# Kernel tuning notes

Hardware: AMD Instinct MI355X
Metric: run time of the kernel (lower is better)

## Reference

```python
import jax, jax.numpy as jnp
import numpy as np

EPS = 1e-12  # torch F.normalize eps

def _l2norm(v, axis):
    n = jnp.sqrt(jnp.sum(v * v, axis=axis, keepdims=True))
    return v / jnp.maximum(n, EPS)

def setup_inputs() -> dict:
    key = jax.random.key(0)
    k1, k2 = jax.random.split(key)
    B, N, D, K = 8, 2048, 128, 64
    x = jax.random.normal(k1, (B, N, D), dtype=jnp.float32)
    std1 = 1.0 / np.sqrt(K * D)
    centroids = jax.random.uniform(k2, (K, D), dtype=jnp.float32, minval=-std1, maxval=std1)
    return {"x": x, "centroids": centroids}

def reference(x, centroids):
    # x: [B, N, D], centroids: [K, D]
    B, N, D = x.shape
    K = centroids.shape[0]
    xn = _l2norm(x, axis=-1)                       # descriptor-wise L2 normalize
    res = xn[:, :, None, :] - centroids[None, None]  # [B, N, K, D]
    dist = jnp.sum(res * res, axis=-1)             # [B, N, K] squared distances
    assign = jax.nn.softmax(dist, axis=-1)         # softmax over clusters (NOTE: positive distances, as in source)
    vlad = jnp.einsum('bnk,bnkd->bkd', assign, res)  # weighted residual sum over N
    vlad = _l2norm(vlad, axis=2)                   # intra-normalization per cluster
    vlad = vlad.reshape(B, K * D)
    vlad = _l2norm(vlad, axis=1)                   # global L2 normalize
    return vlad
```

## Files before the change

### kernel.cpp

```cpp
#include <hip/hip_runtime.h>
#include <math.h>

#define BB 8
#define NN 2048
#define DD 128
#define KK 64
#define PP 32
#define NPB (NN / PP)

__global__ __launch_bounds__(256) void netvlad_k1(
    const float* __restrict__ x, const float* __restrict__ cent,
    float* __restrict__ part_acc, float* __restrict__ part_sA)
{
    const int b    = blockIdx.x >> 5;
    const int p    = blockIdx.x & 31;
    const int t    = threadIdx.x;
    const int kq   = t >> 3;
    const int pr   = t & 7;
    const int dbase = pr * 16;
    const int wave = t >> 6;
    const int lane = t & 63;
    const int half = (t >> 5) & 1;
    const int hl   = t & 31;

    __shared__ float xn[8][DD];
    __shared__ float eL[8][KK];
    __shared__ float rsum[8];

    int off[4];
    #pragma unroll
    for (int jj = 0; jj < 4; ++jj) off[jj] = dbase + (((jj + pr) & 3) << 2);

    float4 cA[4], cB[4];
    float cn2a = 0.f, cn2b = 0.f;
    #pragma unroll
    for (int jj = 0; jj < 4; ++jj) {
        cA[jj] = *(const float4*)(cent + (2 * kq) * DD + off[jj]);
        cB[jj] = *(const float4*)(cent + (2 * kq + 1) * DD + off[jj]);
        cn2a += cA[jj].x*cA[jj].x + cA[jj].y*cA[jj].y + cA[jj].z*cA[jj].z + cA[jj].w*cA[jj].w;
        cn2b += cB[jj].x*cB[jj].x + cB[jj].y*cB[jj].y + cB[jj].z*cB[jj].z + cB[jj].w*cB[jj].w;
    }
    #pragma unroll
    for (int m = 1; m < 8; m <<= 1) {
        cn2a += __shfl_xor(cn2a, m);
        cn2b += __shfl_xor(cn2b, m);
    }

    float4 acc0[4], acc1[4];
    #pragma unroll
    for (int jj = 0; jj < 4; ++jj) {
        acc0[jj] = make_float4(0.f, 0.f, 0.f, 0.f);
        acc1[jj] = make_float4(0.f, 0.f, 0.f, 0.f);
    }
    float sA0 = 0.f, sA1 = 0.f;

    const float* xb = x + ((size_t)b * NN + (size_t)p * NPB) * DD;

    for (int it = 0; it < NPB / 8; ++it) {
        __syncthreads();

        {
            const int i = wave * 2 + half;
            const float* xp = xb + (size_t)(it * 8 + i) * DD + hl * 4;
            float4 v = *(const float4*)xp;
            float ss = v.x*v.x + v.y*v.y + v.z*v.z + v.w*v.w;
            #pragma unroll
            for (int m = 1; m < 32; m <<= 1) ss += __shfl_xor(ss, m);
            const float rn = 1.0f / fmaxf(sqrtf(ss), 1e-12f);
            *(float4*)(&xn[i][hl * 4]) = make_float4(v.x*rn, v.y*rn, v.z*rn, v.w*rn);
        }
        __syncthreads();

        float e0[8], e1[8];
        #pragma unroll
        for (int i = 0; i < 8; ++i) {
            float S0 = 0.f, S1 = 0.f;
            #pragma unroll
            for (int jj = 0; jj < 4; ++jj) {
                float4 v = *(const float4*)(&xn[i][off[jj]]);
                S0 += v.x*cA[jj].x + v.y*cA[jj].y + v.z*cA[jj].z + v.w*cA[jj].w;
                S1 += v.x*cB[jj].x + v.y*cB[jj].y + v.z*cB[jj].z + v.w*cB[jj].w;
            }
            #pragma unroll
            for (int m = 1; m < 8; m <<= 1) {
                S0 += __shfl_xor(S0, m);
                S1 += __shfl_xor(S1, m);
            }
            e0[i] = __expf(cn2a - 2.f * S0);
            e1[i] = __expf(cn2b - 2.f * S1);
            if (pr == 0) *(float2*)(&eL[i][2 * kq]) = make_float2(e0[i], e1[i]);
        }
        __syncthreads();

        #pragma unroll
        for (int rep = 0; rep < 2; ++rep) {
            const int i = wave * 2 + rep;
            float e = eL[i][lane];
            #pragma unroll
            for (int m = 1; m < 64; m <<= 1) e += __shfl_xor(e, m);
            if (lane == 0) rsum[i] = 1.0f / e;
        }
        __syncthreads();

        #pragma unroll
        for (int i = 0; i < 8; ++i) {
            const float r = rsum[i];
            const float a0 = e0[i] * r, a1 = e1[i] * r;
            sA0 += a0; sA1 += a1;
            #pragma unroll
            for (int jj = 0; jj < 4; ++jj) {
                float4 v = *(const float4*)(&xn[i][off[jj]]);
                acc0[jj].x += a0*v.x; acc0[jj].y += a0*v.y; acc0[jj].z += a0*v.z; acc0[jj].w += a0*v.w;
                acc1[jj].x += a1*v.x; acc1[jj].y += a1*v.y; acc1[jj].z += a1*v.z; acc1[jj].w += a1*v.w;
            }
        }
    }

    const size_t base = (size_t)(b * PP + p) * KK * DD;
    #pragma unroll
    for (int jj = 0; jj < 4; ++jj) {
        *(float4*)(part_acc + base + (2 * kq) * DD + off[jj])     = acc0[jj];
        *(float4*)(part_acc + base + (2 * kq + 1) * DD + off[jj]) = acc1[jj];
    }
    if (pr == 0) {
        part_sA[(b * PP + p) * KK + 2 * kq]     = sA0;
        part_sA[(b * PP + p) * KK + 2 * kq + 1] = sA1;
    }
}

__global__ __launch_bounds__(128) void netvlad_k2(
    const float* __restrict__ cent, const float* __restrict__ part_acc,
    const float* __restrict__ part_sA, float* __restrict__ out,
    float* __restrict__ gnorm)
{
    const int b = blockIdx.x >> 6;
    const int k = blockIdx.x & 63;
    const int d = threadIdx.x;

    float sAt = 0.f;
    #pragma unroll
    for (int p = 0; p < PP; ++p) sAt += part_sA[(b * PP + p) * KK + k];

    float v = 0.f;
    #pragma unroll 8
    for (int p = 0; p < PP; ++p)
        v += part_acc[(size_t)(b * PP + p) * KK * DD + k * DD + d];
    v -= cent[k * DD + d] * sAt;

    float ss = v * v;
    #pragma unroll
    for (int m = 1; m < 64; m <<= 1) ss += __shfl_xor(ss, m);
    __shared__ float s2[2];
    if ((d & 63) == 0) s2[d >> 6] = ss;
    __syncthreads();
    const float tot = s2[0] + s2[1];
    const float rn = 1.0f / fmaxf(sqrtf(tot), 1e-12f);
    out[(size_t)b * KK * DD + k * DD + d] = v * rn;

    if (d == 0) atomicAdd(&gnorm[b], tot * rn * rn);
}

__global__ __launch_bounds__(256) void netvlad_k3(
    float* __restrict__ out, const float* __restrict__ gnorm)
{
    const int b = blockIdx.x >> 3;
    const int chunk = blockIdx.x & 7;
    const float rs = 1.0f / fmaxf(sqrtf(gnorm[b]), 1e-12f);
    float4* p = (float4*)(out + (size_t)b * KK * DD) + chunk * 256 + threadIdx.x;
    float4 v = *p;
    v.x *= rs; v.y *= rs; v.z *= rs; v.w *= rs;
    *p = v;
}

extern "C" void kernel_launch(void* const* d_in, const int* in_sizes, int n_in,
                              void* d_out, int out_size, void* d_ws, size_t ws_size,
                              hipStream_t stream) {
    const float* x    = (const float*)d_in[0];
    const float* cent = (const float*)d_in[1];
    float* out = (float*)d_out;

    char* ws = (char*)d_ws;
    float* gnorm    = (float*)ws;
    float* part_sA  = (float*)(ws + 4096);
    float* part_acc = (float*)(ws + 4096 + 65536);

    hipMemsetAsync(gnorm, 0, BB * sizeof(float), stream);

    netvlad_k1<<<dim3(BB * PP), dim3(256), 0, stream>>>(x, cent, part_acc, part_sA);
    netvlad_k2<<<dim3(BB * KK), dim3(128), 0, stream>>>(cent, part_acc, part_sA, out, gnorm);
    netvlad_k3<<<dim3(64), dim3(256), 0, stream>>>(out, gnorm);
}
```

Baseline: 106.3 us.

## Split N across more blocks, vectorize partial reduction, drop global-norm pass

The N dimension is split into 128 partitions instead of 32, so the main kernel launches four times as many blocks, and launch bounds request higher occupancy. The reduction kernel now sums partials with float4 loads, splitting the partition range across four thread groups and combining them through shared memory. The global L2 pass, its atomic and the memset are removed by using a constant 1/8 scale, since each of the 64 intra-normalized clusters has unit norm. In exchange, partial-accumulator traffic grows fourfold, and the constant scale is wrong if any cluster vector has zero norm.

Result: faster. 98.87 us (-7.0%).

```diff
diff --git a/kernel.cpp b/kernel.cpp
--- a/kernel.cpp
+++ b/kernel.cpp
@@ -5,15 +5,15 @@
 #define NN 2048
 #define DD 128
 #define KK 64
-#define PP 32
+#define PP 128
 #define NPB (NN / PP)
 
-__global__ __launch_bounds__(256) void netvlad_k1(
+__global__ __launch_bounds__(256, 4) void netvlad_k1(
     const float* __restrict__ x, const float* __restrict__ cent,
     float* __restrict__ part_acc, float* __restrict__ part_sA)
 {
-    const int b    = blockIdx.x >> 5;
-    const int p    = blockIdx.x & 31;
+    const int b    = blockIdx.x >> 7;
+    const int p    = blockIdx.x & 127;
     const int t    = threadIdx.x;
     const int kq   = t >> 3;
     const int pr   = t & 7;
@@ -130,46 +130,52 @@
 
 __global__ __launch_bounds__(128) void netvlad_k2(
     const float* __restrict__ cent, const float* __restrict__ part_acc,
-    const float* __restrict__ part_sA, float* __restrict__ out,
-    float* __restrict__ gnorm)
+    const float* __restrict__ part_sA, float* __restrict__ out)
 {
-    const int b = blockIdx.x >> 6;
-    const int k = blockIdx.x & 63;
-    const int d = threadIdx.x;
+    const int b  = blockIdx.x >> 6;
+    const int k  = blockIdx.x & 63;
+    const int t  = threadIdx.x;
+    const int d4 = t & 31;
+    const int ps = t >> 5;
 
-    float sAt = 0.f;
-    #pragma unroll
-    for (int p = 0; p < PP; ++p) sAt += part_sA[(b * PP + p) * KK + k];
+    __shared__ float sAL[2];
+    {
+        float sA = part_sA[(b * PP + t) * KK + k];
+        #pragma unroll
+        for (int m = 1; m < 64; m <<= 1) sA += __shfl_xor(sA, m);
+        if ((t & 63) == 0) sAL[t >> 6] = sA;
+    }
 
-    float v = 0.f;
+    float4 acc = make_float4(0.f, 0.f, 0.f, 0.f);
+    const float* base = part_acc + ((size_t)(b * PP) * KK + k) * DD + d4 * 4;
     #pragma unroll 8
-    for (int p = 0; p < PP; ++p)
-        v += part_acc[(size_t)(b * PP + p) * KK * DD + k * DD + d];
-    v -= cent[k * DD + d] * sAt;
+    for (int pp = 0; pp < 32; ++pp) {
+        const float4 v = *(const float4*)(base + (size_t)(ps * 32 + pp) * KK * DD);
+        acc.x += v.x; acc.y += v.y; acc.z += v.z; acc.w += v.w;
+    }
 
-    float ss = v * v;
-    #pragma unroll
-    for (int m = 1; m < 64; m <<= 1) ss += __shfl_xor(ss, m);
-    __shared__ float s2[2];
-    if ((d & 63) == 0) s2[d >> 6] = ss;
+    __shared__ float4 red[4][32];
+    red[ps][d4] = acc;
     __syncthreads();
-    const float tot = s2[0] + s2[1];
-    const float rn = 1.0f / fmaxf(sqrtf(tot), 1e-12f);
-    out[(size_t)b * KK * DD + k * DD + d] = v * rn;
+    const float sAt = sAL[0] + sAL[1];
 
-    if (d == 0) atomicAdd(&gnorm[b], tot * rn * rn);
-}
+    if (t < 32) {
+        float4 v = red[0][t];
+        #pragma unroll
+        for (int s = 1; s < 4; ++s) {
+            v.x += red[s][t].x; v.y += red[s][t].y;
+            v.z += red[s][t].z; v.w += red[s][t].w;
+        }
+        const float4 c = *(const float4*)(cent + k * DD + t * 4);
+        v.x -= c.x * sAt; v.y -= c.y * sAt; v.z -= c.z * sAt; v.w -= c.w * sAt;
 
-__global__ __launch_bounds__(256) void netvlad_k3(
-    float* __restrict__ out, const float* __restrict__ gnorm)
-{
-    const int b = blockIdx.x >> 3;
-    const int chunk = blockIdx.x & 7;
-    const float rs = 1.0f / fmaxf(sqrtf(gnorm[b]), 1e-12f);
-    float4* p = (float4*)(out + (size_t)b * KK * DD) + chunk * 256 + threadIdx.x;
-    float4 v = *p;
-    v.x *= rs; v.y *= rs; v.z *= rs; v.w *= rs;
-    *p = v;
+        float ss = v.x*v.x + v.y*v.y + v.z*v.z + v.w*v.w;
+        #pragma unroll
+        for (int m = 1; m < 32; m <<= 1) ss += __shfl_xor(ss, m);
+        const float rn = 0.125f / fmaxf(sqrtf(ss), 1e-12f);
+        v.x *= rn; v.y *= rn; v.z *= rn; v.w *= rn;
+        *(float4*)(out + ((size_t)b * KK + k) * DD + t * 4) = v;
+    }
 }
 
 extern "C" void kernel_launch(void* const* d_in, const int* in_sizes, int n_in,
@@ -180,13 +186,9 @@
     float* out = (float*)d_out;
 
     char* ws = (char*)d_ws;
-    float* gnorm    = (float*)ws;
-    float* part_sA  = (float*)(ws + 4096);
-    float* part_acc = (float*)(ws + 4096 + 65536);
-
-    hipMemsetAsync(gnorm, 0, BB * sizeof(float), stream);
+    float* part_sA  = (float*)ws;
+    float* part_acc = (float*)(ws + (1 << 19));
 
     netvlad_k1<<<dim3(BB * PP), dim3(256), 0, stream>>>(x, cent, part_acc, part_sA);
-    netvlad_k2<<<dim3(BB * KK), dim3(128), 0, stream>>>(cent, part_acc, part_sA, out, gnorm);
-    netvlad_k3<<<dim3(64), dim3(256), 0, stream>>>(out, gnorm);
+    netvlad_k2<<<dim3(BB * KK), dim3(128), 0, stream>>>(cent, part_acc, part_sA, out);
 }
```
